# Performance work log

Hardware: AMD Instinct MI355X
Metric: run time of the kernel (lower is better)

The kernel has to match this reference:

```python
import jax, jax.numpy as jnp
import numpy as np

T, B, D_IN, D_H = 1024, 128, 256, 256


def setup_inputs() -> dict:
    key = jax.random.key(0)
    ks = jax.random.split(key, 9)
    s_in = 1.0 / np.sqrt(D_IN + D_H)  # torch nn.Linear init scale
    inputs = jax.random.normal(ks[0], (T, B, D_IN), dtype=jnp.float32)
    def lin(kw, kb):
        W = jax.random.uniform(kw, (D_IN + D_H, D_H), jnp.float32, -s_in, s_in)
        b = jax.random.uniform(kb, (D_H,), jnp.float32, -s_in, s_in)
        return W, b
    Wf, bf = lin(ks[1], ks[2])
    Wi, bi = lin(ks[3], ks[4])
    Wg, bg = lin(ks[5], ks[6])
    Wo, bo = lin(ks[7], ks[8])
    return {"inputs": inputs, "Wf": Wf, "bf": bf, "Wi": Wi, "bi": bi,
            "Wg": Wg, "bg": bg, "Wo": Wo, "bo": bo}


def reference(inputs, Wf, bf, Wi, bi, Wg, bg, Wo, bo):
    Bsz = inputs.shape[1]
    h0 = jnp.zeros((Bsz, D_H), inputs.dtype)
    c0 = jnp.zeros((Bsz, D_H), inputs.dtype)

    def step(carry, x):
        hx, cx = carry
        combined = jnp.concatenate([x, hx], axis=1)  # [B, D_IN+D_H]
        f = jax.nn.sigmoid(combined @ Wf + bf)
        i = jax.nn.sigmoid(combined @ Wi + bi)
        g = jnp.tanh(combined @ Wg + bg)
        o = jax.nn.sigmoid(combined @ Wo + bo)
        cx = f * cx + i * g
        hx = o * jnp.tanh(cx)
        return (hx, cx), hx

    (hx, cx), outputs = jax.lax.scan(step, (h0, c0), inputs)
    return outputs, (hx, cx)
```

## Files before the change

kernel.cpp:

```cpp
#include <hip/hip_runtime.h>
#include <hip/hip_bf16.h>

typedef short s16x8 __attribute__((ext_vector_type(8)));
typedef int   i32x4 __attribute__((ext_vector_type(4)));
typedef float f32x4 __attribute__((ext_vector_type(4)));
typedef float f32x2 __attribute__((ext_vector_type(2)));

#define T_STEPS 1024
#define BATCH   128
#define DIN     256
#define DH      256
#define NWG     64
#define NTHREADS 256

static __device__ __forceinline__ short f2bf(float f) {
  return __builtin_bit_cast(short, (__bf16)f);
}
static __device__ __forceinline__ float sigf(float x){ return 1.f/(1.f+__expf(-x)); }
static __device__ __forceinline__ float tanhfast(float x){ return 1.f - 2.f/(1.f+__expf(2.f*x)); }

static __device__ __forceinline__ i32x4 ld16_cc(const void* p){
  i32x4 r; asm volatile("global_load_dwordx4 %0, %1, off sc0 sc1" : "=v"(r) : "v"(p) : "memory"); return r;
}
static __device__ __forceinline__ unsigned ld4_cc(const void* p){
  unsigned r; asm volatile("global_load_dword %0, %1, off sc0 sc1\ns_waitcnt vmcnt(0)" : "=v"(r) : "v"(p) : "memory"); return r;
}
static __device__ __forceinline__ void st4_cc(void* p, unsigned v){
  asm volatile("global_store_dword %0, %1, off sc0 sc1" :: "v"(p), "v"(v) : "memory");
}

static __device__ __forceinline__ s16x8 cvt8(f32x4 a, f32x4 b){
  s16x8 r;
  r[0]=f2bf(a[0]); r[1]=f2bf(a[1]); r[2]=f2bf(a[2]); r[3]=f2bf(a[3]);
  r[4]=f2bf(b[0]); r[5]=f2bf(b[1]); r[6]=f2bf(b[2]); r[7]=f2bf(b[3]);
  return r;
}

__global__ __launch_bounds__(NTHREADS, 1)
void lstm_rc(const float* __restrict__ X,
             const float* __restrict__ Wf, const float* __restrict__ bfv,
             const float* __restrict__ Wi, const float* __restrict__ biv,
             const float* __restrict__ Wg, const float* __restrict__ bgv,
             const float* __restrict__ Wo, const float* __restrict__ bov,
             float* __restrict__ out,
             unsigned short* __restrict__ hbuf,
             unsigned int* __restrict__ flags,
             int needEnd)
{
  const int bid = blockIdx.x;
  const int r   = bid & 7;
  const int csl = bid >> 3;
  const int tid = threadIdx.x;
  const int lane = tid & 63, wv = tid >> 6;
  const int grp = lane >> 4, l15 = lane & 15;
  const int r0 = r * 16;

  __shared__ short bfx[64 * 64 * 8];
  __shared__ float elds[4 * 16 * 36];

  s16x8 bh[2][8];
  {
    const float* Wm[4] = {Wf, Wi, Wg, Wo};
    const int gate = l15 >> 2, jj = l15 & 3;
    const float* Wsrc = Wm[gate];
#pragma unroll
    for (int n2 = 0; n2 < 2; ++n2) {
      const int hc = csl * 32 + (wv * 2 + n2) * 4 + jj;
#pragma unroll
      for (int kk = 0; kk < 16; ++kk) {
        const float* p = Wsrc + (size_t)(kk * 32 + grp * 8) * DH + hc;
        s16x8 f;
#pragma unroll
        for (int s = 0; s < 8; ++s) f[s] = f2bf(p[(size_t)s * DH]);
        if (kk < 8) *(s16x8*)&bfx[(((wv * 2 + n2) * 8 + kk) * 64 + lane) * 8] = f;
        else        bh[n2][kk - 8] = f;
      }
    }
  }

  const int colg = csl * 32 + wv * 8 + 2 * grp;
  float bia[4][2];
  {
    const float* Bv[4] = {bfv, biv, bgv, bov};
#pragma unroll
    for (int g = 0; g < 4; ++g) { bia[g][0] = Bv[g][colg]; bia[g][1] = Bv[g][colg + 1]; }
  }
  __syncthreads();

  f32x4 xr[16];
  {
    const float* xs0 = X + (size_t)(r0 + l15) * DIN + grp * 8;
#pragma unroll
    for (int kk = 0; kk < 8; ++kk) {
      xr[2 * kk]     = *(const f32x4*)(xs0 + kk * 32);
      xr[2 * kk + 1] = *(const f32x4*)(xs0 + kk * 32 + 4);
    }
  }
  f32x4 accx0 = {0.f,0.f,0.f,0.f}, accx1 = {0.f,0.f,0.f,0.f};
#pragma unroll
  for (int kk = 0; kk < 8; ++kk) {
    s16x8 fa = cvt8(xr[2 * kk], xr[2 * kk + 1]);
    s16x8 b0 = *(const s16x8*)&bfx[(((wv * 2 + 0) * 8 + kk) * 64 + lane) * 8];
    s16x8 b1 = *(const s16x8*)&bfx[(((wv * 2 + 1) * 8 + kk) * 64 + lane) * 8];
    accx0 = __builtin_amdgcn_mfma_f32_16x16x32_bf16(fa, b0, accx0, 0, 0, 0);
    accx1 = __builtin_amdgcn_mfma_f32_16x16x32_bf16(fa, b1, accx1, 0, 0, 0);
  }

  unsigned* myflag = flags + (r * 32 + csl);
  const unsigned* pollp = flags + (r * 32 + (lane & 7));
  float* eldsw = &elds[wv * 16 * 36];
  float cs0 = 0.f, cs1 = 0.f, h0s = 0.f, h1s = 0.f;

  for (int t = 0; t < T_STEPS; ++t) {
    while (1) {
      unsigned v = ld4_cc(pollp);
      if (__all((int)(v >= (unsigned)t))) break;
    }
    __builtin_amdgcn_sched_barrier(0);

    const unsigned short* hr = hbuf + (size_t)(t & 1) * (BATCH * DH)
                             + (size_t)(r0 + l15) * DH + grp * 8;
    i32x4 hraw[8];
#pragma unroll
    for (int q = 0; q < 8; ++q) hraw[q] = ld16_cc(hr + q * 32);
    asm volatile("s_waitcnt vmcnt(0)" ::: "memory");
    __builtin_amdgcn_sched_barrier(0);

    f32x4 acc0 = accx0, acc1 = accx1;
#pragma unroll
    for (int q = 0; q < 8; ++q) {
      s16x8 ah = __builtin_bit_cast(s16x8, hraw[q]);
      acc0 = __builtin_amdgcn_mfma_f32_16x16x32_bf16(ah, bh[0][q], acc0, 0, 0, 0);
      acc1 = __builtin_amdgcn_mfma_f32_16x16x32_bf16(ah, bh[1][q], acc1, 0, 0, 0);
    }

#pragma unroll
    for (int rr = 0; rr < 4; ++rr) {
      eldsw[(grp * 4 + rr) * 36 + l15]      = acc0[rr];
      eldsw[(grp * 4 + rr) * 36 + 16 + l15] = acc1[rr];
    }
    asm volatile("s_waitcnt lgkmcnt(0)" ::: "memory");
    __builtin_amdgcn_sched_barrier(0);
    float z0[4], z1[4];
    const int hc0 = 2 * grp, hc1 = 2 * grp + 1;
#pragma unroll
    for (int g = 0; g < 4; ++g) {
      z0[g] = eldsw[l15 * 36 + ((hc0 >> 2) << 4) + 4 * g + (hc0 & 3)];
      z1[g] = eldsw[l15 * 36 + ((hc1 >> 2) << 4) + 4 * g + (hc1 & 3)];
    }

    {
      float zf = z0[0] + bia[0][0], zi = z0[1] + bia[1][0];
      float zg = z0[2] + bia[2][0], zo = z0[3] + bia[3][0];
      cs0 = sigf(zf) * cs0 + sigf(zi) * tanhfast(zg);
      h0s = sigf(zo) * tanhfast(cs0);
    }
    {
      float zf = z1[0] + bia[0][1], zi = z1[1] + bia[1][1];
      float zg = z1[2] + bia[2][1], zo = z1[3] + bia[3][1];
      cs1 = sigf(zf) * cs1 + sigf(zi) * tanhfast(zg);
      h1s = sigf(zo) * tanhfast(cs1);
    }

    const int row = r0 + l15;
    {
      unsigned hpk = (unsigned)(unsigned short)f2bf(h0s)
                   | ((unsigned)(unsigned short)f2bf(h1s) << 16);
      st4_cc(hbuf + (size_t)((t + 1) & 1) * (BATCH * DH)
             + (size_t)row * DH + colg, hpk);
    }
    asm volatile("s_waitcnt vmcnt(0)" ::: "memory");
    __syncthreads();
    if (tid == 0) st4_cc(myflag, (unsigned)(t + 1));

    {
      f32x2 ov; ov[0] = h0s; ov[1] = h1s;
      *(f32x2*)(out + ((size_t)t * BATCH + row) * DH + colg) = ov;
    }
    {
      const int tnx = (t + 1 < T_STEPS) ? t + 1 : T_STEPS - 1;
      const float* xs = X + ((size_t)tnx * BATCH + r0 + l15) * DIN + grp * 8;
#pragma unroll
      for (int kk = 0; kk < 8; ++kk) {
        xr[2 * kk]     = *(const f32x4*)(xs + kk * 32);
        xr[2 * kk + 1] = *(const f32x4*)(xs + kk * 32 + 4);
      }
    }
    accx0 = (f32x4){0.f,0.f,0.f,0.f}; accx1 = (f32x4){0.f,0.f,0.f,0.f};
#pragma unroll
    for (int kk = 0; kk < 8; ++kk) {
      s16x8 fa = cvt8(xr[2 * kk], xr[2 * kk + 1]);
      s16x8 b0 = *(const s16x8*)&bfx[(((wv * 2 + 0) * 8 + kk) * 64 + lane) * 8];
      s16x8 b1 = *(const s16x8*)&bfx[(((wv * 2 + 1) * 8 + kk) * 64 + lane) * 8];
      accx0 = __builtin_amdgcn_mfma_f32_16x16x32_bf16(fa, b0, accx0, 0, 0, 0);
      accx1 = __builtin_amdgcn_mfma_f32_16x16x32_bf16(fa, b1, accx1, 0, 0, 0);
    }
  }

  if (needEnd) {
    if (wv == 0) {
      const unsigned* fp = flags + ((lane >> 3) * 32 + (lane & 7));
      while (ld4_cc(fp) < (unsigned)T_STEPS) __builtin_amdgcn_s_sleep(1);
    }
    __syncthreads();
  }
  {
    const size_t base = (size_t)T_STEPS * BATCH * DH;
    const size_t idx  = (size_t)(r0 + l15) * DH + colg;
    out[base + idx]     = h0s;
    out[base + idx + 1] = h1s;
    out[base + BATCH * DH + idx]     = cs0;
    out[base + BATCH * DH + idx + 1] = cs1;
  }
}

extern "C" void kernel_launch(void* const* d_in, const int* in_sizes, int n_in,
                              void* d_out, int out_size, void* d_ws, size_t ws_size,
                              hipStream_t stream) {
  const float* X   = (const float*)d_in[0];
  const float* Wf  = (const float*)d_in[1];
  const float* bf_ = (const float*)d_in[2];
  const float* Wi  = (const float*)d_in[3];
  const float* bi_ = (const float*)d_in[4];
  const float* Wg  = (const float*)d_in[5];
  const float* bg_ = (const float*)d_in[6];
  const float* Wo  = (const float*)d_in[7];
  const float* bo_ = (const float*)d_in[8];
  float* out = (float*)d_out;

  const size_t hbytes = (size_t)2 * BATCH * DH * 2;
  const size_t fbytes = 2048;
  unsigned short* hbuf;
  unsigned int*   flags;
  int needEnd;
  if (ws_size >= hbytes + fbytes) {
    hbuf  = (unsigned short*)d_ws;
    flags = (unsigned int*)((unsigned char*)d_ws + hbytes);
    needEnd = 0;
    hipMemsetAsync(d_ws, 0, hbytes + fbytes, stream);
  } else {
    unsigned char* tail = (unsigned char*)d_out + (size_t)T_STEPS * BATCH * DH * 4;
    hbuf  = (unsigned short*)tail;
    flags = (unsigned int*)(tail + hbytes);
    needEnd = 1;
    hipMemsetAsync(tail, 0, hbytes + fbytes, stream);
  }

  lstm_rc<<<NWG, NTHREADS, 0, stream>>>(X, Wf, bf_, Wi, bi_, Wg, bg_,
                                        Wo, bo_, out, hbuf, flags, needEnd);
}
```

Baseline: 4.414 ms.

## Use per-wave flags, register-resident weights, and LDS-staged x overlapped with h load

Replaces the per-block __syncthreads plus single flag with per-wave flags, so each wave publishes its h slice as soon as its own store completes, and pollers check 32 flags. All W weights now live in registers instead of splitting the x half into LDS. The input x for step t+1 is converted to bf16 and staged into a double-buffered LDS tile shared by the block. The x-projection MFMAs are issued inside the critical path while the h loads are in flight, rather than after the flag publish. This shortens the inter-block handoff, at the cost of more registers and of x-MFMAs now sitting between the poll and the h-dependent work.

```diff
diff --git a/kernel.cpp b/kernel.cpp
--- a/kernel.cpp
+++ b/kernel.cpp
@@ -13,11 +13,9 @@
 #define NWG     64
 #define NTHREADS 256
 
-static __device__ __forceinline__ short f2bf(float f) {
-  return __builtin_bit_cast(short, (__bf16)f);
-}
+static __device__ __forceinline__ short f2bf(float f){ return __builtin_bit_cast(short,(__bf16)f); }
 static __device__ __forceinline__ float sigf(float x){ return 1.f/(1.f+__expf(-x)); }
-static __device__ __forceinline__ float tanhfast(float x){ return 1.f - 2.f/(1.f+__expf(2.f*x)); }
+static __device__ __forceinline__ float tanhfast(float x){ return 1.f-2.f/(1.f+__expf(2.f*x)); }
 
 static __device__ __forceinline__ i32x4 ld16_cc(const void* p){
   i32x4 r; asm volatile("global_load_dwordx4 %0, %1, off sc0 sc1" : "=v"(r) : "v"(p) : "memory"); return r;
@@ -27,6 +25,9 @@
 }
 static __device__ __forceinline__ void st4_cc(void* p, unsigned v){
   asm volatile("global_store_dword %0, %1, off sc0 sc1" :: "v"(p), "v"(v) : "memory");
+}
+static __device__ __forceinline__ void st8_p(void* p, f32x2 v){
+  asm volatile("global_store_dwordx2 %0, %1, off" :: "v"(p), "v"(v) : "memory");
 }
 
 static __device__ __forceinline__ s16x8 cvt8(f32x4 a, f32x4 b){
@@ -37,28 +38,30 @@
 }
 
 __global__ __launch_bounds__(NTHREADS, 1)
-void lstm_rc(const float* __restrict__ X,
-             const float* __restrict__ Wf, const float* __restrict__ bfv,
-             const float* __restrict__ Wi, const float* __restrict__ biv,
-             const float* __restrict__ Wg, const float* __restrict__ bgv,
-             const float* __restrict__ Wo, const float* __restrict__ bov,
-             float* __restrict__ out,
-             unsigned short* __restrict__ hbuf,
-             unsigned int* __restrict__ flags,
-             int needEnd)
+void lstm_v10(const float* __restrict__ X,
+              const float* __restrict__ Wf, const float* __restrict__ bfv,
+              const float* __restrict__ Wi, const float* __restrict__ biv,
+              const float* __restrict__ Wg, const float* __restrict__ bgv,
+              const float* __restrict__ Wo, const float* __restrict__ bov,
+              float* __restrict__ out,
+              unsigned short* __restrict__ hbuf,
+              unsigned int* __restrict__ flags,
+              int needEnd)
 {
   const int bid = blockIdx.x;
-  const int r   = bid & 7;
+  const int g   = bid & 7;
   const int csl = bid >> 3;
   const int tid = threadIdx.x;
   const int lane = tid & 63, wv = tid >> 6;
   const int grp = lane >> 4, l15 = lane & 15;
-  const int r0 = r * 16;
-
-  __shared__ short bfx[64 * 64 * 8];
+  const int r0 = g * 16;
+
+  __shared__ short bfx_unused[4];
+  __shared__ short a_lds[2 * 32 * 16 * 8];
   __shared__ float elds[4 * 16 * 36];
-
-  s16x8 bh[2][8];
+  (void)bfx_unused;
+
+  s16x8 bfr[2][16];
   {
     const float* Wm[4] = {Wf, Wi, Wg, Wo};
     const int gate = l15 >> 2, jj = l15 & 3;
@@ -72,8 +75,7 @@
         s16x8 f;
 #pragma unroll
         for (int s = 0; s < 8; ++s) f[s] = f2bf(p[(size_t)s * DH]);
-        if (kk < 8) *(s16x8*)&bfx[(((wv * 2 + n2) * 8 + kk) * 64 + lane) * 8] = f;
-        else        bh[n2][kk - 8] = f;
+        bfr[n2][kk] = f;
       }
     }
   }
@@ -83,31 +85,26 @@
   {
     const float* Bv[4] = {bfv, biv, bgv, bov};
 #pragma unroll
-    for (int g = 0; g < 4; ++g) { bia[g][0] = Bv[g][colg]; bia[g][1] = Bv[g][colg + 1]; }
+    for (int q = 0; q < 4; ++q) { bia[q][0] = Bv[q][colg]; bia[q][1] = Bv[q][colg + 1]; }
+  }
+
+  const int xrow = tid & 15, xseg = tid >> 4;
+
+  f32x4 xp0, xp1, xp2, xp3;
+  {
+    const float* xs = X + (size_t)(r0 + xrow) * DIN + xseg * 16;
+    s16x8 lo = cvt8(*(const f32x4*)xs, *(const f32x4*)(xs + 4));
+    s16x8 hi = cvt8(*(const f32x4*)(xs + 8), *(const f32x4*)(xs + 12));
+    *(s16x8*)&a_lds[((2 * xseg + 0) * 16 + xrow) * 8] = lo;
+    *(s16x8*)&a_lds[((2 * xseg + 1) * 16 + xrow) * 8] = hi;
+    const float* xn = X + ((size_t)1 * BATCH + r0 + xrow) * DIN + xseg * 16;
+    xp0 = *(const f32x4*)xn;       xp1 = *(const f32x4*)(xn + 4);
+    xp2 = *(const f32x4*)(xn + 8); xp3 = *(const f32x4*)(xn + 12);
   }
   __syncthreads();
 
-  f32x4 xr[16];
-  {
-    const float* xs0 = X + (size_t)(r0 + l15) * DIN + grp * 8;
-#pragma unroll
-    for (int kk = 0; kk < 8; ++kk) {
-      xr[2 * kk]     = *(const f32x4*)(xs0 + kk * 32);
-      xr[2 * kk + 1] = *(const f32x4*)(xs0 + kk * 32 + 4);
-    }
-  }
-  f32x4 accx0 = {0.f,0.f,0.f,0.f}, accx1 = {0.f,0.f,0.f,0.f};
-#pragma unroll
-  for (int kk = 0; kk < 8; ++kk) {
-    s16x8 fa = cvt8(xr[2 * kk], xr[2 * kk + 1]);
-    s16x8 b0 = *(const s16x8*)&bfx[(((wv * 2 + 0) * 8 + kk) * 64 + lane) * 8];
-    s16x8 b1 = *(const s16x8*)&bfx[(((wv * 2 + 1) * 8 + kk) * 64 + lane) * 8];
-    accx0 = __builtin_amdgcn_mfma_f32_16x16x32_bf16(fa, b0, accx0, 0, 0, 0);
-    accx1 = __builtin_amdgcn_mfma_f32_16x16x32_bf16(fa, b1, accx1, 0, 0, 0);
-  }
-
-  unsigned* myflag = flags + (r * 32 + csl);
-  const unsigned* pollp = flags + (r * 32 + (lane & 7));
+  unsigned* myflag = flags + (g * 32 + csl * 4 + wv);
+  const unsigned* pollp = flags + (g * 32 + (lane & 31));
   float* eldsw = &elds[wv * 16 * 36];
   float cs0 = 0.f, cs1 = 0.f, h0s = 0.f, h1s = 0.f;
 
@@ -123,15 +120,30 @@
     i32x4 hraw[8];
 #pragma unroll
     for (int q = 0; q < 8; ++q) hraw[q] = ld16_cc(hr + q * 32);
+
+    {
+      short* ab = a_lds + ((t + 1) & 1) * (32 * 16 * 8);
+      s16x8 lo = cvt8(xp0, xp1), hi = cvt8(xp2, xp3);
+      *(s16x8*)&ab[((2 * xseg + 0) * 16 + xrow) * 8] = lo;
+      *(s16x8*)&ab[((2 * xseg + 1) * 16 + xrow) * 8] = hi;
+    }
+
+    const short* ar = a_lds + (t & 1) * (32 * 16 * 8);
+    f32x4 acc0 = {0.f,0.f,0.f,0.f}, acc1 = {0.f,0.f,0.f,0.f};
+#pragma unroll
+    for (int kk = 0; kk < 8; ++kk) {
+      s16x8 a = *(const s16x8*)&ar[((kk * 4 + grp) * 16 + l15) * 8];
+      acc0 = __builtin_amdgcn_mfma_f32_16x16x32_bf16(a, bfr[0][kk], acc0, 0, 0, 0);
+      acc1 = __builtin_amdgcn_mfma_f32_16x16x32_bf16(a, bfr[1][kk], acc1, 0, 0, 0);
+    }
+
     asm volatile("s_waitcnt vmcnt(0)" ::: "memory");
     __builtin_amdgcn_sched_barrier(0);
-
-    f32x4 acc0 = accx0, acc1 = accx1;
 #pragma unroll
     for (int q = 0; q < 8; ++q) {
       s16x8 ah = __builtin_bit_cast(s16x8, hraw[q]);
-      acc0 = __builtin_amdgcn_mfma_f32_16x16x32_bf16(ah, bh[0][q], acc0, 0, 0, 0);
-      acc1 = __builtin_amdgcn_mfma_f32_16x16x32_bf16(ah, bh[1][q], acc1, 0, 0, 0);
+      acc0 = __builtin_amdgcn_mfma_f32_16x16x32_bf16(ah, bfr[0][8 + q], acc0, 0, 0, 0);
+      acc1 = __builtin_amdgcn_mfma_f32_16x16x32_bf16(ah, bfr[1][8 + q], acc1, 0, 0, 0);
     }
 
 #pragma unroll
@@ -144,11 +156,10 @@
     float z0[4], z1[4];
     const int hc0 = 2 * grp, hc1 = 2 * grp + 1;
 #pragma unroll
-    for (int g = 0; g < 4; ++g) {
-      z0[g] = eldsw[l15 * 36 + ((hc0 >> 2) << 4) + 4 * g + (hc0 & 3)];
-      z1[g] = eldsw[l15 * 36 + ((hc1 >> 2) << 4) + 4 * g + (hc1 & 3)];
-    }
-
+    for (int q = 0; q < 4; ++q) {
+      z0[q] = eldsw[l15 * 36 + ((hc0 >> 2) << 4) + 4 * q + (hc0 & 3)];
+      z1[q] = eldsw[l15 * 36 + ((hc1 >> 2) << 4) + 4 * q + (hc1 & 3)];
+    }
     {
       float zf = z0[0] + bia[0][0], zi = z0[1] + bia[1][0];
       float zg = z0[2] + bia[2][0], zo = z0[3] + bia[3][0];
@@ -168,40 +179,24 @@
                    | ((unsigned)(unsigned short)f2bf(h1s) << 16);
       st4_cc(hbuf + (size_t)((t + 1) & 1) * (BATCH * DH)
              + (size_t)row * DH + colg, hpk);
-    }
-    asm volatile("s_waitcnt vmcnt(0)" ::: "memory");
-    __syncthreads();
-    if (tid == 0) st4_cc(myflag, (unsigned)(t + 1));
-
-    {
       f32x2 ov; ov[0] = h0s; ov[1] = h1s;
-      *(f32x2*)(out + ((size_t)t * BATCH + row) * DH + colg) = ov;
-    }
-    {
-      const int tnx = (t + 1 < T_STEPS) ? t + 1 : T_STEPS - 1;
-      const float* xs = X + ((size_t)tnx * BATCH + r0 + l15) * DIN + grp * 8;
-#pragma unroll
-      for (int kk = 0; kk < 8; ++kk) {
-        xr[2 * kk]     = *(const f32x4*)(xs + kk * 32);
-        xr[2 * kk + 1] = *(const f32x4*)(xs + kk * 32 + 4);
-      }
-    }
-    accx0 = (f32x4){0.f,0.f,0.f,0.f}; accx1 = (f32x4){0.f,0.f,0.f,0.f};
-#pragma unroll
-    for (int kk = 0; kk < 8; ++kk) {
-      s16x8 fa = cvt8(xr[2 * kk], xr[2 * kk + 1]);
-      s16x8 b0 = *(const s16x8*)&bfx[(((wv * 2 + 0) * 8 + kk) * 64 + lane) * 8];
-      s16x8 b1 = *(const s16x8*)&bfx[(((wv * 2 + 1) * 8 + kk) * 64 + lane) * 8];
-      accx0 = __builtin_amdgcn_mfma_f32_16x16x32_bf16(fa, b0, accx0, 0, 0, 0);
-      accx1 = __builtin_amdgcn_mfma_f32_16x16x32_bf16(fa, b1, accx1, 0, 0, 0);
+      st8_p(out + ((size_t)t * BATCH + row) * DH + colg, ov);
+    }
+
+    asm volatile("s_waitcnt vmcnt(1)" ::: "memory");
+    if (lane == 0) st4_cc(myflag, (unsigned)(t + 1));
+
+    {
+      const int tp = (t + 2 < T_STEPS) ? t + 2 : T_STEPS - 1;
+      const float* xs = X + ((size_t)tp * BATCH + r0 + xrow) * DIN + xseg * 16;
+      xp0 = *(const f32x4*)xs;       xp1 = *(const f32x4*)(xs + 4);
+      xp2 = *(const f32x4*)(xs + 8); xp3 = *(const f32x4*)(xs + 12);
     }
   }
 
   if (needEnd) {
-    if (wv == 0) {
-      const unsigned* fp = flags + ((lane >> 3) * 32 + (lane & 7));
-      while (ld4_cc(fp) < (unsigned)T_STEPS) __builtin_amdgcn_s_sleep(1);
-    }
+    const unsigned* fp = flags + tid;
+    while (ld4_cc(fp) < (unsigned)T_STEPS) __builtin_amdgcn_s_sleep(1);
     __syncthreads();
   }
   {
@@ -229,7 +224,7 @@
   float* out = (float*)d_out;
 
   const size_t hbytes = (size_t)2 * BATCH * DH * 2;
-  const size_t fbytes = 2048;
+  const size_t fbytes = 1024;
   unsigned short* hbuf;
   unsigned int*   flags;
   int needEnd;
@@ -246,6 +241,6 @@
     hipMemsetAsync(tail, 0, hbytes + fbytes, stream);
   }
 
-  lstm_rc<<<NWG, NTHREADS, 0, stream>>>(X, Wf, bf_, Wi, bi_, Wg, bg_,
-                                        Wo, bo_, out, hbuf, flags, needEnd);
-}
+  lstm_v10<<<NWG, NTHREADS, 0, stream>>>(X, Wf, bf_, Wi, bi_, Wg, bg_,
+                                         Wo, bo_, out, hbuf, flags, needEnd);
+}
```

New measurement: 4.302 ms. 2.5% less time.
